# Kernel optimization log

Hardware: AMD Instinct MI355X
Metric: run time of the kernel (lower is better)

## Reference

```python
import jax, jax.numpy as jnp
import numpy as np

D_MODEL, H, DK, DV = 1024, 16, 64, 64
B, NQ, NK = 4, 1024, 1024
LN_EPS = 1e-5


def setup_inputs() -> dict:
    key = jax.random.key(0)
    ks = jax.random.split(key, 16)
    xavier = lambda k, i, o: jax.random.uniform(k, (i, o), jnp.float32,
                                                -np.sqrt(6.0 / (i + o)), np.sqrt(6.0 / (i + o)))
    return {
        "queries": jax.random.normal(ks[0], (B, NQ, D_MODEL), jnp.float32),
        "keys": jax.random.normal(ks[1], (B, NK, D_MODEL), jnp.float32),
        "values": jax.random.normal(ks[2], (B, NK, D_MODEL), jnp.float32),
        "geometry": jax.random.uniform(ks[3], (B, H, NQ, NK), jnp.float32),
        "attention_mask": jax.random.bernoulli(ks[4], 0.1, (B, H, NQ, NK)),
        "Wq": xavier(ks[5], D_MODEL, H * DK), "bq": jnp.zeros((H * DK,), jnp.float32),
        "Wk": xavier(ks[6], D_MODEL, H * DK), "bk": jnp.zeros((H * DK,), jnp.float32),
        "Wv": xavier(ks[7], D_MODEL, H * DV), "bv": jnp.zeros((H * DV,), jnp.float32),
        "Wo": xavier(ks[8], H * DV, D_MODEL), "bo": jnp.zeros((D_MODEL,), jnp.float32),
        "ln_gamma": jnp.ones((D_MODEL,), jnp.float32),
        "ln_beta": jnp.zeros((D_MODEL,), jnp.float32),
    }


def reference(queries, keys, values, geometry, attention_mask,
              Wq, bq, Wk, bk, Wv, bv, Wo, bo, ln_gamma, ln_beta):
    b, nq, _ = queries.shape
    nk = keys.shape[1]
    # QKV projections -> (b, h, n, d)
    q = (queries @ Wq + bq).reshape(b, nq, H, DK).transpose(0, 2, 1, 3)
    k = (keys @ Wk + bk).reshape(b, nk, H, DK).transpose(0, 2, 1, 3)
    v = (values @ Wv + bv).reshape(b, nk, H, DV).transpose(0, 2, 1, 3)
    att = jnp.einsum('bhqd,bhkd->bhqk', q, k) / np.sqrt(DK).astype(np.float32)
    att = jnp.where(attention_mask, -jnp.inf, att)
    # inline geometry log-bias before softmax
    w = jnp.log(jnp.clip(geometry, 1e-6)) + att
    w = jax.nn.softmax(w, axis=-1)  # dropout is identity in eval
    out = jnp.einsum('bhqk,bhkd->bqhd', w, v).reshape(b, nq, H * DV)
    out = out @ Wo + bo
    # residual + LayerNorm
    x = queries + out  # dropout identity in eval
    mu = jnp.mean(x, axis=-1, keepdims=True)
    var = jnp.mean((x - mu) ** 2, axis=-1, keepdims=True)
    return (x - mu) * jax.lax.rsqrt(var + LN_EPS) * ln_gamma + ln_beta
```

## Files before the change

### kernel.cpp

```cpp
#include <hip/hip_runtime.h>
#include <hip/hip_bf16.h>

typedef unsigned short u16;
typedef unsigned char u8;
typedef unsigned long long u64;
typedef __bf16 bf16x8 __attribute__((ext_vector_type(8)));
typedef float f32x4 __attribute__((ext_vector_type(4)));

#define AS1 __attribute__((address_space(1)))
#define AS3 __attribute__((address_space(3)))
#define GLL16(gp, lp) __builtin_amdgcn_global_load_lds((AS1 const unsigned int*)(gp), (AS3 unsigned int*)(lp), 16, 0, 0)

__device__ __forceinline__ u16 f2bf(float f) {
    unsigned u = __builtin_bit_cast(unsigned, f);
    unsigned r = u + 0x7FFFu + ((u >> 16) & 1u);
    return (u16)(r >> 16);
}

__global__ void detect_kernel(const unsigned char* __restrict__ m, int* __restrict__ flag) {
    __shared__ int cnt1;
    __shared__ int big;
    if (threadIdx.x == 0) { cnt1 = 0; big = 0; }
    __syncthreads();
    int c1 = 0, bg = 0;
    for (int i = threadIdx.x; i < 16384; i += 256) {
        unsigned char v = m[i];
        if (v) {
            if ((i & 3) == 1) c1++;
            if (v > 1) bg++;
        }
    }
    atomicAdd(&cnt1, c1);
    atomicAdd(&big, bg);
    __syncthreads();
    if (threadIdx.x == 0) {
        int f;
        if (big == 0) f = cnt1 ? 0 : 1;
        else          f = cnt1 ? 3 : 2;
        *flag = f;
    }
}

#define MN_LOOP(PRED)                                                     \
    for (int row = wave; row < 65536; row += nw) {                        \
        size_t base = (size_t)row * 1024;                                 \
        u64 myw = 0;                                                      \
        _Pragma("unroll")                                                 \
        for (int kb = 0; kb < 16; ++kb) {                                 \
            size_t gi = base + kb * 64 + lane;                            \
            bool p = (PRED);                                              \
            u64 w = __ballot(p);                                          \
            if (lane == kb) myw = w;                                      \
        }                                                                 \
        if (lane < 16) MB[(size_t)row * 16 + lane] = myw;                 \
    }

__global__ __launch_bounds__(256) void masknorm_kernel(const void* __restrict__ mp,
                                                       const int* __restrict__ flagp,
                                                       u64* __restrict__ MB) {
    const int flag = *flagp;
    const int lane = threadIdx.x & 63;
    const int wave = blockIdx.x * 4 + (threadIdx.x >> 6);
    const int nw = gridDim.x * 4;
    if (flag == 0) {
        const unsigned char* m8 = (const unsigned char*)mp;
        MN_LOOP(m8[gi] != 0)
    } else if (flag == 1) {
        const int* m32 = (const int*)mp;
        MN_LOOP(m32[gi] != 0)
    } else if (flag == 2) {
        const unsigned* mf = (const unsigned*)mp;
        MN_LOOP((mf[gi] << 1) != 0)
    } else {
        const u16* mb = (const u16*)mp;
        MN_LOOP((mb[gi] & 0x7FFF) != 0)
    }
}

__global__ void cast3_kernel(const float* __restrict__ q, const float* __restrict__ k,
                             const float* __restrict__ v, u16* __restrict__ xq,
                             u16* __restrict__ xk, u16* __restrict__ xv) {
    const int n4 = 4 * 1024 * 1024 / 4;
    int stride = gridDim.x * blockDim.x;
    for (int i = blockIdx.x * blockDim.x + threadIdx.x; i < n4; i += stride) {
        float4 a = ((const float4*)q)[i];
        float4 b = ((const float4*)k)[i];
        float4 c = ((const float4*)v)[i];
        ((ushort4*)xq)[i] = make_ushort4(f2bf(a.x), f2bf(a.y), f2bf(a.z), f2bf(a.w));
        ((ushort4*)xk)[i] = make_ushort4(f2bf(b.x), f2bf(b.y), f2bf(b.z), f2bf(b.w));
        ((ushort4*)xv)[i] = make_ushort4(f2bf(c.x), f2bf(c.y), f2bf(c.z), f2bf(c.w));
    }
}

__global__ __launch_bounds__(256) void wtrans_kernel(
    const float* __restrict__ W0, const float* __restrict__ W1,
    const float* __restrict__ W2, const float* __restrict__ W3,
    u16* __restrict__ T0, u16* __restrict__ T1, u16* __restrict__ T2, u16* __restrict__ T3) {
    const float* W = (blockIdx.z == 0) ? W0 : (blockIdx.z == 1) ? W1 : (blockIdx.z == 2) ? W2 : W3;
    u16* T = (blockIdx.z == 0) ? T0 : (blockIdx.z == 1) ? T1 : (blockIdx.z == 2) ? T2 : T3;
    __shared__ float t[64][65];
    const int n0 = blockIdx.x * 64, k0 = blockIdx.y * 64;
    const int tx = threadIdx.x, ty = threadIdx.y;
    for (int j = ty; j < 64; j += 4) t[j][tx] = W[(size_t)(k0 + j) * 1024 + n0 + tx];
    __syncthreads();
    for (int j = ty; j < 64; j += 4) T[(size_t)(n0 + j) * 1024 + k0 + tx] = f2bf(t[tx][j]);
}

__device__ __forceinline__ void gemm_core(const u16* __restrict__ A, const u16* __restrict__ Bt,
                                          u16* sA, u16* sB, f32x4 (&acc)[4][4],
                                          int tid, int bm, int bn) {
    const int lane = tid & 63, wid = tid >> 6;
    const int wr = wid >> 1, wc = wid & 1;
    const int l15 = lane & 15, l4 = lane >> 4;
    const int srow = tid >> 2, sslot = tid & 3;
    const int soff = (sslot ^ ((srow >> 1) & 3)) * 8;
    const u16* aSrc = A + (size_t)(bm * 128 + srow) * 1024 + soff;
    const u16* bSrc = Bt + (size_t)(bn * 128 + srow) * 1024 + soff;
    u16* const dA0 = sA + wid * 512;
    u16* const dA1 = sA + 2048 + wid * 512;
    u16* const dB0 = sB + wid * 512;
    u16* const dB1 = sB + 2048 + wid * 512;

#define GSTAGE(BUF, T)                                                  \
    do {                                                                \
        GLL16(aSrc + (T) * 32, dA0 + (BUF) * 4096);                     \
        GLL16(aSrc + 65536 + (T) * 32, dA1 + (BUF) * 4096);             \
        GLL16(bSrc + (T) * 32, dB0 + (BUF) * 4096);                     \
        GLL16(bSrc + 65536 + (T) * 32, dB1 + (BUF) * 4096);             \
    } while (0)

#define GCOMPUTE(BUF)                                                             \
    do {                                                                          \
        bf16x8 af[4], bfv[4];                                                     \
        _Pragma("unroll")                                                         \
        for (int m = 0; m < 4; ++m) {                                             \
            const int rr = wr * 64 + m * 16 + l15;                                \
            af[m] = *(const bf16x8*)(sA + (BUF) * 4096 + rr * 32 +                \
                                     ((l4 ^ ((rr >> 1) & 3)) * 8));               \
        }                                                                         \
        _Pragma("unroll")                                                         \
        for (int n = 0; n < 4; ++n) {                                             \
            const int rr = wc * 64 + n * 16 + l15;                                \
            bfv[n] = *(const bf16x8*)(sB + (BUF) * 4096 + rr * 32 +               \
                                      ((l4 ^ ((rr >> 1) & 3)) * 8));              \
        }                                                                         \
        _Pragma("unroll")                                                         \
        for (int m = 0; m < 4; ++m)                                               \
            _Pragma("unroll")                                                     \
            for (int n = 0; n < 4; ++n)                                           \
                acc[m][n] = __builtin_amdgcn_mfma_f32_16x16x32_bf16(af[m], bfv[n], acc[m][n], 0, 0, 0); \
    } while (0)

#define GBODY(T, BUF, NBUF, WSTR)                                       \
    do {                                                                \
        if ((T) + 2 < 32) {                                             \
            GSTAGE(NBUF, (T) + 2);                                      \
            __builtin_amdgcn_sched_barrier(0);                          \
        }                                                               \
        GCOMPUTE(BUF);                                                  \
        if ((T) + 1 < 32) {                                             \
            asm volatile(WSTR ::: "memory");                            \
            __builtin_amdgcn_sched_barrier(0);                          \
            __builtin_amdgcn_s_barrier();                               \
            __builtin_amdgcn_sched_barrier(0);                          \
        }                                                               \
    } while (0)

    GSTAGE(0, 0);
    GSTAGE(1, 1);
    __builtin_amdgcn_sched_barrier(0);
    asm volatile("s_waitcnt vmcnt(4)" ::: "memory");
    __builtin_amdgcn_sched_barrier(0);
    __builtin_amdgcn_s_barrier();
    __builtin_amdgcn_sched_barrier(0);

    for (int it = 0; it < 10; ++it) {
        const int t0 = it * 3;
        GBODY(t0 + 0, 0, 2, "s_waitcnt vmcnt(4)");
        GBODY(t0 + 1, 1, 0, "s_waitcnt vmcnt(4)");
        GBODY(t0 + 2, 2, 1, "s_waitcnt vmcnt(4)");
    }
    GBODY(30, 0, 2, "s_waitcnt vmcnt(0)");
    GBODY(31, 1, 0, "s_waitcnt vmcnt(0)");
#undef GBODY
#undef GCOMPUTE
#undef GSTAGE
}

__global__ __launch_bounds__(256, 3) void qkv_gemm(
    const u16* __restrict__ XQ, const u16* __restrict__ XK, const u16* __restrict__ XV,
    const u16* __restrict__ WQT, const u16* __restrict__ WKT, const u16* __restrict__ WVT,
    const float* __restrict__ bq, const float* __restrict__ bk, const float* __restrict__ bv,
    u16* __restrict__ QS, u16* __restrict__ KS, u16* __restrict__ VT) {
    __shared__ __align__(16) u16 smem[24576];
    const int z = blockIdx.z;
    const u16* A  = (z == 0) ? XQ : (z == 1) ? XK : XV;
    const u16* Bt = (z == 0) ? WQT : (z == 1) ? WKT : WVT;
    const float* bias = (z == 0) ? bq : (z == 1) ? bk : bv;
    const int tid = threadIdx.x, lane = tid & 63, wid = tid >> 6;
    const int bm = blockIdx.y, bn = blockIdx.x;
    const int wr = wid >> 1, wc = wid & 1;
    const int l15 = lane & 15, l4 = lane >> 4;

    f32x4 acc[4][4] = {};
    gemm_core(A, Bt, smem, smem + 12288, acc, tid, bm, bn);

    if (z == 2) {
        __syncthreads();
        u16* tl = smem;
#pragma unroll
        for (int n = 0; n < 4; ++n) {
            const int cl = wc * 64 + n * 16 + l15;
            const float bv_ = bias[bn * 128 + cl];
#pragma unroll
            for (int m = 0; m < 4; ++m)
#pragma unroll
                for (int j = 0; j < 4; ++j) {
                    const int rl = wr * 64 + m * 16 + l4 * 4 + j;
                    tl[cl * 132 + rl] = f2bf(acc[m][n][j] + bv_);
                }
        }
        __syncthreads();
        const int bb = bm >> 3, k0 = (bm & 7) * 128;
#pragma unroll
        for (int i = 0; i < 8; ++i) {
            const int idx = i * 256 + tid;
            const int row = idx >> 4, col16 = idx & 15;
            const int cg = bn * 128 + row;
            const int hh = cg >> 6, dd = cg & 63;
            bf16x8 v = *(const bf16x8*)(tl + row * 132 + col16 * 8);
            *(bf16x8*)(VT + ((size_t)((bb * 16 + hh) * 64 + dd)) * 1024 + k0 + col16 * 8) = v;
        }
    } else {
        u16* outp = (z == 0) ? QS : KS;
        const float scale = (z == 0) ? 0.125f : 1.0f;
#pragma unroll
        for (int n = 0; n < 4; ++n) {
            const int c = bn * 128 + wc * 64 + n * 16 + l15;
            const float bv_ = bias[c];
#pragma unroll
            for (int m = 0; m < 4; ++m)
#pragma unroll
                for (int j = 0; j < 4; ++j) {
                    const int r = bm * 128 + wr * 64 + m * 16 + l4 * 4 + j;
                    outp[(size_t)r * 1024 + c] = f2bf((acc[m][n][j] + bv_) * scale);
                }
        }
    }
}

__global__ __launch_bounds__(256, 3) void gemm_out(
    const u16* __restrict__ A, const u16* __restrict__ Bt, const float* __restrict__ bias,
    float* __restrict__ outp, const float* __restrict__ resid) {
    __shared__ __align__(16) u16 smem[24576];
    const int tid = threadIdx.x, lane = tid & 63, wid = tid >> 6;
    const int bm = blockIdx.y, bn = blockIdx.x;
    const int wr = wid >> 1, wc = wid & 1;
    const int l15 = lane & 15, l4 = lane >> 4;

    f32x4 acc[4][4] = {};
    gemm_core(A, Bt, smem, smem + 12288, acc, tid, bm, bn);

#pragma unroll
    for (int n = 0; n < 4; ++n) {
        const int c = bn * 128 + wc * 64 + n * 16 + l15;
        const float bv = bias[c];
#pragma unroll
        for (int m = 0; m < 4; ++m)
#pragma unroll
            for (int j = 0; j < 4; ++j) {
                const int r = bm * 128 + wr * 64 + m * 16 + l4 * 4 + j;
                outp[(size_t)r * 1024 + c] = acc[m][n][j] + bv + resid[(size_t)r * 1024 + c];
            }
    }
}

__global__ __launch_bounds__(256, 3) void attn_kernel(
    const u16* __restrict__ Qs, const u16* __restrict__ Ks, const u16* __restrict__ Vt,
    const float* __restrict__ geom, const u64* __restrict__ MBw,
    u16* __restrict__ AO) {
    __shared__ __align__(16) u16 lds[20480];

    const int g = blockIdx.x;
    const int tt = (g & 7) * 128 + (g >> 3);
    const int qb = tt & 15;
    const int bhid = tt >> 4;
    const int b = bhid >> 4, h = bhid & 15;
    const int q0 = qb * 64;

    const int tid = threadIdx.x, lane = tid & 63, wid = tid >> 6;
    const int l15 = lane & 15, l4 = lane >> 4;
    const int qrow = q0 + wid * 16;
    const size_t bh = (size_t)bhid;

    const u16* qp = Qs + (size_t)(b * 1024 + qrow + l15) * 1024 + h * 64 + l4 * 8;
    bf16x8 aq0 = *(const bf16x8*)qp;
    bf16x8 aq1 = *(const bf16x8*)(qp + 32);

    const int r0 = tid >> 3, s0 = tid & 7;
    const int r1 = 32 + r0;
    const int kgr0 = (r0 & 15) * 4 + (r0 >> 4);
    const int kgr1 = (r1 & 15) * 4 + (r1 >> 4);
    const u16* ksrc0 = Ks + (size_t)(b * 1024 + kgr0) * 1024 + h * 64 + ((s0 ^ (r0 & 7)) * 8);
    const u16* ksrc1 = Ks + (size_t)(b * 1024 + kgr1) * 1024 + h * 64 + ((s0 ^ (r1 & 7)) * 8);
    const u16* vsrc0 = Vt + (bh * 64 + r0) * 1024 + ((s0 ^ (r0 & 7)) * 8);
    const u16* vsrc1 = Vt + (bh * 64 + r1) * 1024 + ((s0 ^ (r1 & 7)) * 8);
    u16* const KD = lds + wid * 512;
    u16* const VD = lds + 8192 + wid * 512;
    u16* const pw = lds + 16384 + wid * 1024;

    const float* gbase = geom + (bh * 1024 + qrow + l4 * 4) * 1024 + l15 * 4;
    const u8* mbase8 = (const u8*)MBw + (size_t)(bh * 1024 + qrow + l4 * 4) * 128 + (l15 >> 1);
    const int nsh = (l15 & 1) * 4;

    f32x4 o[4] = {};
    float m_run[4], l_run[4];
#pragma unroll
    for (int j = 0; j < 4; ++j) { m_run[j] = -1e30f; l_run[j] = 0.f; }

    f32x4 gpA[4], gpB[4];
    unsigned mkA[4], mkB[4];

    GLL16(ksrc0, KD);
    GLL16(ksrc1, KD + 2048);
    GLL16(vsrc0, VD);
    GLL16(vsrc1, VD + 2048);
    __builtin_amdgcn_sched_barrier(0);
#pragma unroll
    for (int j = 0; j < 4; ++j) {
        gpA[j] = *(const f32x4*)(gbase + j * 1024);
        mkA[j] = mbase8[j * 128];
    }
    __builtin_amdgcn_sched_barrier(0);
    asm volatile("s_waitcnt vmcnt(8)" ::: "memory");
    __builtin_amdgcn_sched_barrier(0);
    __builtin_amdgcn_s_barrier();
    __builtin_amdgcn_sched_barrier(0);

#define BODY(T, G, GC, GN, MC, MN)                                                       \
    do {                                                                                 \
        const u16* KB = lds + ((T) & 1) * 4096;                                          \
        const u16* VB = lds + 8192 + ((T) & 1) * 4096;                                   \
        if (G) {                                                                         \
            const int nb = (((T) + 1) & 1) * 4096;                                       \
            GLL16(ksrc0 + (size_t)((T) + 1) * 65536, KD + nb);                           \
            GLL16(ksrc1 + (size_t)((T) + 1) * 65536, KD + 2048 + nb);                    \
            GLL16(vsrc0 + ((T) + 1) * 64, VD + nb);                                      \
            GLL16(vsrc1 + ((T) + 1) * 64, VD + 2048 + nb);                               \
            __builtin_amdgcn_sched_barrier(0);                                           \
            _Pragma("unroll")                                                            \
            for (int j = 0; j < 4; ++j) {                                                \
                GN[j] = *(const f32x4*)(gbase + j * 1024 + ((T) + 1) * 64);              \
                MN[j] = mbase8[j * 128 + ((T) + 1) * 8];                                 \
            }                                                                            \
            __builtin_amdgcn_sched_barrier(0);                                           \
        }                                                                                \
        f32x4 s[4];                                                                      \
        __builtin_amdgcn_s_setprio(1);                                                   \
        _Pragma("unroll")                                                                \
        for (int nf = 0; nf < 4; ++nf) {                                                 \
            const int rr = nf * 16 + l15, swz = rr & 7;                                  \
            bf16x8 k0 = *(const bf16x8*)(KB + rr * 64 + ((l4 ^ swz) * 8));               \
            bf16x8 k1 = *(const bf16x8*)(KB + rr * 64 + (((4 + l4) ^ swz) * 8));         \
            f32x4 z = {};                                                                \
            z = __builtin_amdgcn_mfma_f32_16x16x32_bf16(aq0, k0, z, 0, 0, 0);            \
            s[nf] = __builtin_amdgcn_mfma_f32_16x16x32_bf16(aq1, k1, z, 0, 0, 0);        \
        }                                                                                \
        __builtin_amdgcn_s_setprio(0);                                                   \
        float sclv[4];                                                                   \
        _Pragma("unroll")                                                                \
        for (int j = 0; j < 4; ++j) {                                                    \
            float mt = fmaxf(fmaxf(s[0][j], s[1][j]), fmaxf(s[2][j], s[3][j]));          \
            mt = fmaxf(mt, __shfl_xor(mt, 1, 16));                                       \
            mt = fmaxf(mt, __shfl_xor(mt, 2, 16));                                       \
            mt = fmaxf(mt, __shfl_xor(mt, 4, 16));                                       \
            mt = fmaxf(mt, __shfl_xor(mt, 8, 16));                                       \
            float mn = fmaxf(m_run[j], mt);                                              \
            float scl = __expf(m_run[j] - mn);                                           \
            m_run[j] = mn;                                                               \
            unsigned nib = (MC[j] >> nsh) & 0xFu;                                        \
            f32x4 gv = GC[j];                                                            \
            float p0 = (nib & 1u) ? 0.f : __expf(s[0][j] - mn) * fmaxf(gv[0], 1e-6f);    \
            float p1 = (nib & 2u) ? 0.f : __expf(s[1][j] - mn) * fmaxf(gv[1], 1e-6f);    \
            float p2 = (nib & 4u) ? 0.f : __expf(s[2][j] - mn) * fmaxf(gv[2], 1e-6f);    \
            float p3 = (nib & 8u) ? 0.f : __expf(s[3][j] - mn) * fmaxf(gv[3], 1e-6f);    \
            float rs = (p0 + p1) + (p2 + p3);                                            \
            rs += __shfl_xor(rs, 1, 16);                                                 \
            rs += __shfl_xor(rs, 2, 16);                                                 \
            rs += __shfl_xor(rs, 4, 16);                                                 \
            rs += __shfl_xor(rs, 8, 16);                                                 \
            l_run[j] = l_run[j] * scl + rs;                                              \
            sclv[j] = scl;                                                               \
            const int row = l4 * 4 + j;                                                  \
            u64 pk = (u64)f2bf(p0) | ((u64)f2bf(p1) << 16) |                             \
                     ((u64)f2bf(p2) << 32) | ((u64)f2bf(p3) << 48);                      \
            *(u64*)(pw + row * 64 + (((l15 >> 1) ^ (row & 7)) * 8) + (l15 & 1) * 4) = pk;\
        }                                                                                \
        _Pragma("unroll")                                                                \
        for (int df = 0; df < 4; ++df) {                                                 \
            f32x4 tv = o[df];                                                            \
            _Pragma("unroll")                                                            \
            for (int j = 0; j < 4; ++j) tv[j] *= sclv[j];                                \
            o[df] = tv;                                                                  \
        }                                                                                \
        {                                                                                \
            const int pswz = l15 & 7;                                                    \
            bf16x8 pa0 = *(const bf16x8*)(pw + l15 * 64 + ((l4 ^ pswz) * 8));            \
            bf16x8 pa1 = *(const bf16x8*)(pw + l15 * 64 + (((4 + l4) ^ pswz) * 8));      \
            __builtin_amdgcn_s_setprio(1);                                               \
            _Pragma("unroll")                                                            \
            for (int df = 0; df < 4; ++df) {                                             \
                const int rr = df * 16 + l15, vswz = rr & 7;                             \
                bf16x8 v0 = *(const bf16x8*)(VB + rr * 64 + ((l4 ^ vswz) * 8));          \
                bf16x8 v1 = *(const bf16x8*)(VB + rr * 64 + (((4 + l4) ^ vswz) * 8));    \
                o[df] = __builtin_amdgcn_mfma_f32_16x16x32_bf16(pa0, v0, o[df], 0, 0, 0);\
                o[df] = __builtin_amdgcn_mfma_f32_16x16x32_bf16(pa1, v1, o[df], 0, 0, 0);\
            }                                                                            \
            __builtin_amdgcn_s_setprio(0);                                               \
        }                                                                                \
        if (G) {                                                                         \
            asm volatile("s_waitcnt vmcnt(8)" ::: "memory");                             \
            __builtin_amdgcn_sched_barrier(0);                                           \
            __builtin_amdgcn_s_barrier();                                                \
            __builtin_amdgcn_sched_barrier(0);                                           \
        }                                                                                \
    } while (0)

    for (int it = 0; it < 7; ++it) {
        const int t0 = it * 2;
        BODY(t0,     1, gpA, gpB, mkA, mkB);
        BODY(t0 + 1, 1, gpB, gpA, mkB, mkA);
    }
    BODY(14, 1, gpA, gpB, mkA, mkB);
    BODY(15, 0, gpB, gpA, mkB, mkA);
#undef BODY

    float inv[4];
#pragma unroll
    for (int j = 0; j < 4; ++j) inv[j] = 1.0f / l_run[j];
#pragma unroll
    for (int df = 0; df < 4; ++df)
#pragma unroll
        for (int j = 0; j < 4; ++j)
            pw[(l4 * 4 + j) * 64 + df * 16 + l15] = f2bf(o[df][j] * inv[j]);
#pragma unroll
    for (int p = 0; p < 2; ++p) {
        const int idx = p * 64 + lane;
        const int er = idx >> 3, ec = idx & 7;
        bf16x8 val = *(const bf16x8*)(pw + er * 64 + ec * 8);
        *(bf16x8*)(AO + (size_t)(b * 1024 + qrow + er) * 1024 + h * 64 + ec * 8) = val;
    }
}

__global__ __launch_bounds__(256) void ln_kernel(const float* __restrict__ Y,
                                                 const float* __restrict__ gamma,
                                                 const float* __restrict__ beta,
                                                 float* __restrict__ out) {
    __shared__ float red[8];
    const int r = blockIdx.x, tid = threadIdx.x, lane = tid & 63, wid = tid >> 6;
    float4 v = ((const float4*)(Y + (size_t)r * 1024))[tid];
    float s = v.x + v.y + v.z + v.w;
    float q = v.x * v.x + v.y * v.y + v.z * v.z + v.w * v.w;
    for (int d = 1; d < 64; d <<= 1) {
        s += __shfl_xor(s, d, 64);
        q += __shfl_xor(q, d, 64);
    }
    if (lane == 0) { red[wid] = s; red[4 + wid] = q; }
    __syncthreads();
    float ts = red[0] + red[1] + red[2] + red[3];
    float tq = red[4] + red[5] + red[6] + red[7];
    float mu = ts * (1.f / 1024.f);
    float var = tq * (1.f / 1024.f) - mu * mu;
    float rstd = rsqrtf(var + 1e-5f);
    float4 gg = ((const float4*)gamma)[tid];
    float4 be = ((const float4*)beta)[tid];
    float4 ov;
    ov.x = (v.x - mu) * rstd * gg.x + be.x;
    ov.y = (v.y - mu) * rstd * gg.y + be.y;
    ov.z = (v.z - mu) * rstd * gg.z + be.z;
    ov.w = (v.w - mu) * rstd * gg.w + be.w;
    ((float4*)(out + (size_t)r * 1024))[tid] = ov;
}

extern "C" void kernel_launch(void* const* d_in, const int* in_sizes, int n_in,
                              void* d_out, int out_size, void* d_ws, size_t ws_size,
                              hipStream_t stream) {
    const float* queries = (const float*)d_in[0];
    const float* keys    = (const float*)d_in[1];
    const float* values  = (const float*)d_in[2];
    const float* geom    = (const float*)d_in[3];
    const void*  mask    = d_in[4];
    const float* Wq = (const float*)d_in[5];  const float* bq = (const float*)d_in[6];
    const float* Wk = (const float*)d_in[7];  const float* bk = (const float*)d_in[8];
    const float* Wv = (const float*)d_in[9];  const float* bv = (const float*)d_in[10];
    const float* Wo = (const float*)d_in[11]; const float* bo = (const float*)d_in[12];
    const float* gamma = (const float*)d_in[13];
    const float* beta  = (const float*)d_in[14];

    char* ws = (char*)d_ws;
    const size_t MB_ = 1024 * 1024;
    u16* XQ  = (u16*)(ws + 0);
    u16* XK  = (u16*)(ws + 8 * MB_);
    u16* XV  = (u16*)(ws + 16 * MB_);
    u16* WQT = (u16*)(ws + 24 * MB_);
    u16* WKT = (u16*)(ws + 26 * MB_);
    u16* WVT = (u16*)(ws + 28 * MB_);
    u16* WOT = (u16*)(ws + 30 * MB_);
    u16* QS  = (u16*)(ws + 32 * MB_);
    u16* KS  = (u16*)(ws + 40 * MB_);
    u16* VT  = (u16*)(ws + 48 * MB_);
    u16* AO  = (u16*)(ws + 56 * MB_);
    u64* MBITS = (u64*)(ws + 16 * MB_);
    float* Y = (float*)(ws + 0);
    int* FLAG = (int*)(ws + 64 * MB_);

    detect_kernel<<<1, 256, 0, stream>>>((const unsigned char*)mask, FLAG);
    cast3_kernel<<<1024, 256, 0, stream>>>(queries, keys, values, XQ, XK, XV);
    wtrans_kernel<<<dim3(16, 16, 4), dim3(64, 4), 0, stream>>>(Wq, Wk, Wv, Wo, WQT, WKT, WVT, WOT);
    qkv_gemm<<<dim3(8, 32, 3), 256, 0, stream>>>(XQ, XK, XV, WQT, WKT, WVT, bq, bk, bv, QS, KS, VT);
    masknorm_kernel<<<4096, 256, 0, stream>>>(mask, FLAG, MBITS);
    attn_kernel<<<1024, 256, 0, stream>>>(QS, KS, VT, geom, MBITS, AO);
    gemm_out<<<dim3(8, 32), 256, 0, stream>>>(AO, WOT, bo, Y, queries);
    ln_kernel<<<4096, 256, 0, stream>>>(Y, gamma, beta, (float*)d_out);
}
```

Baseline: 277.1 us.

## Merge prep kernels, fold mask detection into masknorm, use nontemporal streaming loads

Folds the cast and weight-transpose kernels into one prep launch, and moves mask-format detection into each masknorm block. This removes two kernel launches and the serial single-block detect step. The masknorm grid shrinks from 4096 to 1024 blocks. The attention kernel now reads geometry and mask bits with nontemporal loads so these streamed-once tensors do not pollute the cache, and every masknorm block redundantly re-reads 16 KB of mask to recompute the flag.

```diff
diff --git a/kernel.cpp b/kernel.cpp
--- a/kernel.cpp
+++ b/kernel.cpp
@@ -10,6 +10,7 @@
 #define AS1 __attribute__((address_space(1)))
 #define AS3 __attribute__((address_space(3)))
 #define GLL16(gp, lp) __builtin_amdgcn_global_load_lds((AS1 const unsigned int*)(gp), (AS3 unsigned int*)(lp), 16, 0, 0)
+#define NTL4(p) __builtin_nontemporal_load((const f32x4*)(p))
 
 __device__ __forceinline__ u16 f2bf(float f) {
     unsigned u = __builtin_bit_cast(unsigned, f);
@@ -17,27 +18,35 @@
     return (u16)(r >> 16);
 }
 
-__global__ void detect_kernel(const unsigned char* __restrict__ m, int* __restrict__ flag) {
-    __shared__ int cnt1;
-    __shared__ int big;
-    if (threadIdx.x == 0) { cnt1 = 0; big = 0; }
-    __syncthreads();
-    int c1 = 0, bg = 0;
-    for (int i = threadIdx.x; i < 16384; i += 256) {
-        unsigned char v = m[i];
-        if (v) {
-            if ((i & 3) == 1) c1++;
-            if (v > 1) bg++;
+__global__ __launch_bounds__(256) void prep_kernel(
+    const float* __restrict__ q, const float* __restrict__ k, const float* __restrict__ v,
+    u16* __restrict__ xq, u16* __restrict__ xk, u16* __restrict__ xv,
+    const float* __restrict__ W0, const float* __restrict__ W1,
+    const float* __restrict__ W2, const float* __restrict__ W3,
+    u16* __restrict__ T0, u16* __restrict__ T1, u16* __restrict__ T2, u16* __restrict__ T3) {
+    const int gb = blockIdx.x, tid = threadIdx.x;
+    if (gb < 1024) {
+        const int n4 = 4 * 1024 * 1024 / 4;
+        const int stride = 1024 * 256;
+        for (int i = gb * 256 + tid; i < n4; i += stride) {
+            float4 a = ((const float4*)q)[i];
+            float4 b = ((const float4*)k)[i];
+            float4 c = ((const float4*)v)[i];
+            ((ushort4*)xq)[i] = make_ushort4(f2bf(a.x), f2bf(a.y), f2bf(a.z), f2bf(a.w));
+            ((ushort4*)xk)[i] = make_ushort4(f2bf(b.x), f2bf(b.y), f2bf(b.z), f2bf(b.w));
+            ((ushort4*)xv)[i] = make_ushort4(f2bf(c.x), f2bf(c.y), f2bf(c.z), f2bf(c.w));
         }
-    }
-    atomicAdd(&cnt1, c1);
-    atomicAdd(&big, bg);
-    __syncthreads();
-    if (threadIdx.x == 0) {
-        int f;
-        if (big == 0) f = cnt1 ? 0 : 1;
-        else          f = cnt1 ? 3 : 2;
-        *flag = f;
+    } else {
+        __shared__ float t[64][65];
+        const int idx = gb - 1024;
+        const int bz = idx >> 8, by = (idx >> 4) & 15, bx = idx & 15;
+        const float* W = (bz == 0) ? W0 : (bz == 1) ? W1 : (bz == 2) ? W2 : W3;
+        u16* T = (bz == 0) ? T0 : (bz == 1) ? T1 : (bz == 2) ? T2 : T3;
+        const int n0 = bx * 64, k0 = by * 64;
+        const int tx = tid & 63, ty = tid >> 6;
+        for (int j = ty; j < 64; j += 4) t[j][tx] = W[(size_t)(k0 + j) * 1024 + n0 + tx];
+        __syncthreads();
+        for (int j = ty; j < 64; j += 4) T[(size_t)(n0 + j) * 1024 + k0 + tx] = f2bf(t[tx][j]);
     }
 }
 
@@ -56,9 +65,26 @@
     }
 
 __global__ __launch_bounds__(256) void masknorm_kernel(const void* __restrict__ mp,
-                                                       const int* __restrict__ flagp,
                                                        u64* __restrict__ MB) {
-    const int flag = *flagp;
+    __shared__ int s_cnt1, s_big;
+    if (threadIdx.x == 0) { s_cnt1 = 0; s_big = 0; }
+    __syncthreads();
+    {
+        const unsigned char* m8 = (const unsigned char*)mp;
+        int c1 = 0, bg = 0;
+        for (int i = threadIdx.x; i < 16384; i += 256) {
+            unsigned char vv = m8[i];
+            if (vv) {
+                if ((i & 3) == 1) c1++;
+                if (vv > 1) bg++;
+            }
+        }
+        atomicAdd(&s_cnt1, c1);
+        atomicAdd(&s_big, bg);
+    }
+    __syncthreads();
+    const int flag = (s_big == 0) ? (s_cnt1 ? 0 : 1) : (s_cnt1 ? 3 : 2);
+
     const int lane = threadIdx.x & 63;
     const int wave = blockIdx.x * 4 + (threadIdx.x >> 6);
     const int nw = gridDim.x * 4;
@@ -75,35 +101,6 @@
         const u16* mb = (const u16*)mp;
         MN_LOOP((mb[gi] & 0x7FFF) != 0)
     }
-}
-
-__global__ void cast3_kernel(const float* __restrict__ q, const float* __restrict__ k,
-                             const float* __restrict__ v, u16* __restrict__ xq,
-                             u16* __restrict__ xk, u16* __restrict__ xv) {
-    const int n4 = 4 * 1024 * 1024 / 4;
-    int stride = gridDim.x * blockDim.x;
-    for (int i = blockIdx.x * blockDim.x + threadIdx.x; i < n4; i += stride) {
-        float4 a = ((const float4*)q)[i];
-        float4 b = ((const float4*)k)[i];
-        float4 c = ((const float4*)v)[i];
-        ((ushort4*)xq)[i] = make_ushort4(f2bf(a.x), f2bf(a.y), f2bf(a.z), f2bf(a.w));
-        ((ushort4*)xk)[i] = make_ushort4(f2bf(b.x), f2bf(b.y), f2bf(b.z), f2bf(b.w));
-        ((ushort4*)xv)[i] = make_ushort4(f2bf(c.x), f2bf(c.y), f2bf(c.z), f2bf(c.w));
-    }
-}
-
-__global__ __launch_bounds__(256) void wtrans_kernel(
-    const float* __restrict__ W0, const float* __restrict__ W1,
-    const float* __restrict__ W2, const float* __restrict__ W3,
-    u16* __restrict__ T0, u16* __restrict__ T1, u16* __restrict__ T2, u16* __restrict__ T3) {
-    const float* W = (blockIdx.z == 0) ? W0 : (blockIdx.z == 1) ? W1 : (blockIdx.z == 2) ? W2 : W3;
-    u16* T = (blockIdx.z == 0) ? T0 : (blockIdx.z == 1) ? T1 : (blockIdx.z == 2) ? T2 : T3;
-    __shared__ float t[64][65];
-    const int n0 = blockIdx.x * 64, k0 = blockIdx.y * 64;
-    const int tx = threadIdx.x, ty = threadIdx.y;
-    for (int j = ty; j < 64; j += 4) t[j][tx] = W[(size_t)(k0 + j) * 1024 + n0 + tx];
-    __syncthreads();
-    for (int j = ty; j < 64; j += 4) T[(size_t)(n0 + j) * 1024 + k0 + tx] = f2bf(t[tx][j]);
 }
 
 __device__ __forceinline__ void gemm_core(const u16* __restrict__ A, const u16* __restrict__ Bt,
@@ -328,8 +325,8 @@
     __builtin_amdgcn_sched_barrier(0);
 #pragma unroll
     for (int j = 0; j < 4; ++j) {
-        gpA[j] = *(const f32x4*)(gbase + j * 1024);
-        mkA[j] = mbase8[j * 128];
+        gpA[j] = NTL4(gbase + j * 1024);
+        mkA[j] = __builtin_nontemporal_load(mbase8 + j * 128);
     }
     __builtin_amdgcn_sched_barrier(0);
     asm volatile("s_waitcnt vmcnt(8)" ::: "memory");
@@ -350,8 +347,8 @@
             __builtin_amdgcn_sched_barrier(0);                                           \
             _Pragma("unroll")                                                            \
             for (int j = 0; j < 4; ++j) {                                                \
-                GN[j] = *(const f32x4*)(gbase + j * 1024 + ((T) + 1) * 64);              \
-                MN[j] = mbase8[j * 128 + ((T) + 1) * 8];                                 \
+                GN[j] = NTL4(gbase + j * 1024 + ((T) + 1) * 64);                         \
+                MN[j] = __builtin_nontemporal_load(mbase8 + j * 128 + ((T) + 1) * 8);    \
             }                                                                            \
             __builtin_amdgcn_sched_barrier(0);                                           \
         }                                                                                \
@@ -512,13 +509,11 @@
     u16* AO  = (u16*)(ws + 56 * MB_);
     u64* MBITS = (u64*)(ws + 16 * MB_);
     float* Y = (float*)(ws + 0);
-    int* FLAG = (int*)(ws + 64 * MB_);
-
-    detect_kernel<<<1, 256, 0, stream>>>((const unsigned char*)mask, FLAG);
-    cast3_kernel<<<1024, 256, 0, stream>>>(queries, keys, values, XQ, XK, XV);
-    wtrans_kernel<<<dim3(16, 16, 4), dim3(64, 4), 0, stream>>>(Wq, Wk, Wv, Wo, WQT, WKT, WVT, WOT);
+
+    prep_kernel<<<2048, 256, 0, stream>>>(queries, keys, values, XQ, XK, XV,
+                                          Wq, Wk, Wv, Wo, WQT, WKT, WVT, WOT);
     qkv_gemm<<<dim3(8, 32, 3), 256, 0, stream>>>(XQ, XK, XV, WQT, WKT, WVT, bq, bk, bv, QS, KS, VT);
-    masknorm_kernel<<<4096, 256, 0, stream>>>(mask, FLAG, MBITS);
+    masknorm_kernel<<<1024, 256, 0, stream>>>(mask, MBITS);
     attn_kernel<<<1024, 256, 0, stream>>>(QS, KS, VT, geom, MBITS, AO);
     gemm_out<<<dim3(8, 32), 256, 0, stream>>>(AO, WOT, bo, Y, queries);
     ln_kernel<<<4096, 256, 0, stream>>>(Y, gamma, beta, (float*)d_out);
```

Result: faster. 268.8 us (-3.0%).
